# Kernel tuning notes

Measured on AMD Instinct MI355X. Metric: run time of the kernel, lower is better.

The kernel has to match this reference:

```python
import jax, jax.numpy as jnp
import numpy as np

SCALE = 1.0 / (100.0 ** 0.5)  # module hard-codes QK / sqrt(100)


def setup_inputs() -> dict:
    key = jax.random.key(0)
    k1, k2, k3 = jax.random.split(key, 3)
    B, S, D = 8, 2048, 512
    head_size = 64
    x = jax.random.normal(k1, (B, S, D), dtype=jnp.float32)
    kernel = jax.random.normal(k2, (3, D, head_size), dtype=jnp.float32) * 0.02
    dense = jax.random.normal(k3, (D, D), dtype=jnp.float32) * 0.02
    return {"x": x, "kernel": kernel, "dense": dense, "heads": 8}


def reference(x, kernel, dense, heads):
    # All heads use the SAME kernel slices in the original loop, so each
    # iteration produces an identical V; compute once and tile.
    WQ = jnp.einsum('bsd,dh->bsh', x, kernel[0])  # [B,S,Hd]
    WK = jnp.einsum('bsd,dh->bsh', x, kernel[1])
    WV = jnp.einsum('bsd,dh->bsh', x, kernel[2])
    scores = jnp.einsum('bqh,bkh->bqk', WQ, WK) * SCALE  # [B,S,S]
    attn = jax.nn.softmax(scores, axis=-1)
    V = jnp.einsum('bqk,bkh->bqh', attn, WV)  # [B,S,Hd]
    out = jnp.tile(V, (1, 1, heads))  # concat of identical heads -> [B,S,heads*Hd]
    return jnp.einsum('bsf,fo->bso', out, dense)
```

## Files before the change

kernel.cpp:

```cpp
#include <hip/hip_runtime.h>
#include <math.h>


typedef __bf16 bf16;
typedef __bf16 bf16x4v __attribute__((ext_vector_type(4)));
typedef __bf16 bf16x8v __attribute__((ext_vector_type(8)));
typedef float f32x4 __attribute__((ext_vector_type(4)));

namespace {
constexpr int kS = 2048;
constexpr int kD = 512;
constexpr int kRows = 16384;
}

#define MFMA16(a, b, c) __builtin_amdgcn_mfma_f32_16x16x32_bf16((a), (b), (c), 0, 0, 0)

__global__ __launch_bounds__(256) void prep_kernel(const float* __restrict__ w,
                                                   const float* __restrict__ dense,
                                                   bf16* __restrict__ wtg,
                                                   bf16* __restrict__ drt) {
  int idx = blockIdx.x * 256 + threadIdx.x;
  if (idx < 98304) {
    int mat = idx >> 15, rem = idx & 32767;
    int n = rem >> 9, k = rem & 511;
    wtg[idx] = (bf16)w[mat * 32768 + k * 64 + n];
  } else {
    int e = idx - 98304;
    int o = e >> 6, j = e & 63;
    float s = 0.f;
#pragma unroll
    for (int h = 0; h < 8; ++h) s += dense[(size_t)(h * 64 + j) * kD + o];
    drt[e] = (bf16)s;
  }
}

__global__ __launch_bounds__(256) void proj_kernel(const float* __restrict__ x,
                                                   const bf16* __restrict__ wtg,
                                                   bf16* __restrict__ wq,
                                                   bf16* __restrict__ wk,
                                                   bf16* __restrict__ wvt) {
  const int bt = blockIdx.x;
  const int tid = threadIdx.x;
  const int w = tid >> 6, tx = tid & 15, quad = (tid >> 4) & 3;
  const int row0 = bt * 64;

  __shared__ bf16 Xs[64 * 72];
  __shared__ bf16 Wts[3 * 64 * 72];

  f32x4 acc[3][4];
#pragma unroll
  for (int m = 0; m < 3; ++m)
#pragma unroll
    for (int nt = 0; nt < 4; ++nt) acc[m][nt] = (f32x4){0.f, 0.f, 0.f, 0.f};

  for (int k0 = 0; k0 < kD; k0 += 64) {
    __syncthreads();
#pragma unroll
    for (int p = 0; p < 4; ++p) {
      int i4 = tid + p * 256;
      int r = i4 >> 4, c4 = (i4 & 15) * 4;
      float4 f = *(const float4*)&x[(size_t)(row0 + r) * kD + k0 + c4];
      bf16x4v h = {(bf16)f.x, (bf16)f.y, (bf16)f.z, (bf16)f.w};
      *(bf16x4v*)&Xs[r * 72 + c4] = h;
    }
#pragma unroll
    for (int p = 0; p < 6; ++p) {
      int cc = tid + p * 256;
      int mat = cc >> 9, rem = cc & 511;
      int n = rem >> 3, c8 = (rem & 7) * 8;
      *(uint4*)&Wts[(mat * 64 + n) * 72 + c8] =
          *(const uint4*)&wtg[(size_t)mat * 32768 + (size_t)n * 512 + k0 + c8];
    }
    __syncthreads();
#pragma unroll
    for (int s = 0; s < 2; ++s) {
      bf16x8v a = *(bf16x8v*)&Xs[(w * 16 + tx) * 72 + s * 32 + quad * 8];
#pragma unroll
      for (int m = 0; m < 3; ++m)
#pragma unroll
        for (int nt = 0; nt < 4; ++nt) {
          bf16x8v bfr =
              *(bf16x8v*)&Wts[(m * 64 + nt * 16 + tx) * 72 + s * 32 + quad * 8];
          acc[m][nt] = MFMA16(a, bfr, acc[m][nt]);
        }
    }
  }

#pragma unroll
  for (int nt = 0; nt < 4; ++nt)
#pragma unroll
    for (int r = 0; r < 4; ++r) {
      int row_g = row0 + w * 16 + quad * 4 + r;
      int col = nt * 16 + tx;
      wq[(size_t)row_g * 64 + col] = (bf16)acc[0][nt][r];
      wk[(size_t)row_g * 64 + col] = (bf16)acc[1][nt][r];
    }
  __syncthreads();
  bf16* Vt = Xs;
#pragma unroll
  for (int nt = 0; nt < 4; ++nt)
#pragma unroll
    for (int r = 0; r < 4; ++r)
      Vt[(nt * 16 + tx) * 72 + (w * 16 + quad * 4 + r)] = (bf16)acc[2][nt][r];
  __syncthreads();
#pragma unroll
  for (int p = 0; p < 2; ++p) {
    int c = tid + p * 256;
    int v = c >> 3, seg = c & 7;
    *(uint4*)&wvt[(size_t)v * kRows + row0 + seg * 8] =
        *(uint4*)&Vt[v * 72 + seg * 8];
  }
}

__global__ __launch_bounds__(512, 4) void flash_kernel(
    const bf16* __restrict__ wq, const bf16* __restrict__ wk,
    const bf16* __restrict__ wvt, const bf16* __restrict__ drt,
    float* __restrict__ out) {
  const int bid = blockIdx.x;
  const int b = bid & 7, qb = bid >> 3;
  const int q0 = qb * 32;
  const int tid = threadIdx.x;
  const int w = tid >> 6, lane = tid & 63, tx = tid & 15, quad = (tid >> 4) & 3;

  __shared__ __align__(16) char lds[65536];
  __shared__ float Lsh[256];
  __shared__ __align__(16) bf16 vob[32 * 64];
  bf16* Ksw = (bf16*)(lds + w * 8192);
  bf16* Psw = Ksw;
  bf16* Vtw = (bf16*)(lds + w * 8192 + 4096);

  const bf16* wqb = wq + (size_t)(b * kS) * 64;
  const bf16* wkb = wk + (size_t)(b * kS) * 64;
  const bf16* wvb = wvt + b * kS;

  const int kc0 = (quad ^ (tx & 7)) * 8;
  const int kc1 = ((4 + quad) ^ (tx & 7)) * 8;
  const int h2 = (tx ^ (tx >> 2)) & 3;

  bf16x8v aq[2][2];
#pragma unroll
  for (int rt = 0; rt < 2; ++rt)
#pragma unroll
    for (int s = 0; s < 2; ++s)
      aq[rt][s] = *(const bf16x8v*)&wqb[(size_t)(q0 + rt * 16 + tx) * 64 +
                                        s * 32 + quad * 8];

  f32x4 oacc[2][4];
#pragma unroll
  for (int rt = 0; rt < 2; ++rt)
#pragma unroll
    for (int nt = 0; nt < 4; ++nt) oacc[rt][nt] = (f32x4){0.f, 0.f, 0.f, 0.f};
  float lsum[2][4] = {};

  const int ksr = lane >> 3, kslc = lane & 7;
  const int vsv = lane >> 2, vsck = lane & 3;

  for (int t = 0; t < 8; ++t) {
    const int k0 = (t * 8 + w) * 32;
#pragma unroll
    for (int j = 0; j < 4; ++j) {
      int r = ksr + j * 8;
      *(uint4*)&Ksw[r * 64 + ((kslc ^ (r & 7)) * 8)] =
          *(const uint4*)&wkb[(size_t)(k0 + r) * 64 + kslc * 8];
      int v = vsv + j * 16;
      *(uint4*)&Vtw[v * 32 + ((vsck ^ ((v ^ (v >> 2)) & 3)) * 8)] =
          *(const uint4*)&wvb[(size_t)v * kRows + k0 + vsck * 8];
    }

#pragma unroll
    for (int nt = 0; nt < 2; ++nt) {
      int krow = nt * 16 + tx;
      bf16x8v b0 = *(bf16x8v*)&Ksw[krow * 64 + kc0];
      bf16x8v b1 = *(bf16x8v*)&Ksw[krow * 64 + kc1];
#pragma unroll
      for (int rt = 0; rt < 2; ++rt) {
        f32x4 z = (f32x4){0.f, 0.f, 0.f, 0.f};
        z = MFMA16(aq[rt][0], b0, z);
        z = MFMA16(aq[rt][1], b1, z);
#pragma unroll
        for (int r = 0; r < 4; ++r) {
          float p = __expf(z[r] * 0.1f);
          lsum[rt][r] += p;
          int q = rt * 16 + quad * 4 + r;
          int chunk = nt * 2 + (tx >> 3);
          Psw[q * 32 + ((chunk ^ (r ^ quad)) * 8) + (tx & 7)] = (bf16)p;
        }
      }
    }

#pragma unroll
    for (int rt = 0; rt < 2; ++rt) {
      bf16x8v pa = *(bf16x8v*)&Psw[(rt * 16 + tx) * 32 + ((quad ^ h2) * 8)];
#pragma unroll
      for (int nt = 0; nt < 4; ++nt) {
        bf16x8v vb = *(bf16x8v*)&Vtw[(nt * 16 + tx) * 32 + ((quad ^ h2) * 8)];
        oacc[rt][nt] = MFMA16(pa, vb, oacc[rt][nt]);
      }
    }
  }

  __syncthreads();
  float* myO = (float*)(lds + w * 8192);
  float* myL = Lsh + w * 32;
#pragma unroll
  for (int rt = 0; rt < 2; ++rt)
#pragma unroll
    for (int nt = 0; nt < 4; ++nt)
#pragma unroll
      for (int r = 0; r < 4; ++r)
        myO[(rt * 16 + quad * 4 + r) * 64 + nt * 16 + tx] = oacc[rt][nt][r];
#pragma unroll
  for (int rt = 0; rt < 2; ++rt)
#pragma unroll
    for (int r = 0; r < 4; ++r) {
      float v = lsum[rt][r];
#pragma unroll
      for (int m = 1; m < 16; m <<= 1) v += __shfl_xor(v, m, 64);
      if (tx == 0) myL[rt * 16 + quad * 4 + r] = v;
    }
  __syncthreads();

#pragma unroll
  for (int p = 0; p < 4; ++p) {
    int e = tid + p * 512;
    int row = e >> 6, col = e & 63;
    float s = 0.f, lt = 0.f;
#pragma unroll
    for (int wv = 0; wv < 8; ++wv) {
      s += ((const float*)(lds + wv * 8192))[e];
      lt += Lsh[wv * 32 + row];
    }
    vob[row * 64 + (((col >> 3) ^ (row & 7)) * 8) + (col & 7)] = (bf16)(s / lt);
  }
  __syncthreads();

  bf16x8v av[2][2];
#pragma unroll
  for (int rt = 0; rt < 2; ++rt) {
    av[rt][0] = *(bf16x8v*)&vob[(rt * 16 + tx) * 64 + kc0];
    av[rt][1] = *(bf16x8v*)&vob[(rt * 16 + tx) * 64 + kc1];
  }

  float* OutS = (float*)lds;
#pragma unroll
  for (int c = 0; c < 2; ++c) {
    if (c) __syncthreads();
#pragma unroll
    for (int i = 0; i < 2; ++i) {
      const int ct = c * 16 + w * 2 + i;
      bf16x8v bd0 =
          *(const bf16x8v*)&drt[(size_t)(ct * 16 + tx) * 64 + quad * 8];
      bf16x8v bd1 =
          *(const bf16x8v*)&drt[(size_t)(ct * 16 + tx) * 64 + 32 + quad * 8];
#pragma unroll
      for (int rt = 0; rt < 2; ++rt) {
        f32x4 z = (f32x4){0.f, 0.f, 0.f, 0.f};
        z = MFMA16(av[rt][0], bd0, z);
        z = MFMA16(av[rt][1], bd1, z);
#pragma unroll
        for (int r = 0; r < 4; ++r)
          OutS[(rt * 16 + quad * 4 + r) * 260 + (w * 2 + i) * 16 + tx] = z[r];
      }
    }
    __syncthreads();
#pragma unroll
    for (int p = 0; p < 4; ++p) {
      int e = tid + p * 512;
      int row = e >> 6, seg = e & 63;
      *(float4*)&out[(size_t)(b * kS + q0 + row) * kD + c * 256 + seg * 4] =
          *(float4*)&OutS[row * 260 + seg * 4];
    }
  }
}

extern "C" void kernel_launch(void* const* d_in, const int* in_sizes, int n_in,
                              void* d_out, int out_size, void* d_ws,
                              size_t ws_size, hipStream_t stream) {
  const float* x = (const float*)d_in[0];
  const float* w = (const float*)d_in[1];
  const float* dense = (const float*)d_in[2];
  float* out = (float*)d_out;

  bf16* wq = (bf16*)d_ws;
  bf16* wk = wq + (size_t)kRows * 64;
  bf16* wvt = wk + (size_t)kRows * 64;
  bf16* wtg = wvt + (size_t)kRows * 64;
  bf16* drt = wtg + 98304;

  prep_kernel<<<512, 256, 0, stream>>>(w, dense, wtg, drt);
  proj_kernel<<<256, 256, 0, stream>>>(x, wtg, wq, wk, wvt);
  flash_kernel<<<512, 512, 0, stream>>>(wq, wk, wvt, drt, out);
}
```

Before: 137.7 us.

## Tile prep transposes, widen proj blocks, register-prefetch loads in proj and flash

The prep kernel now transposes the weights through a shared-memory tile and reduces the dense heads in registers, using 32 blocks instead of 512. The projection kernel runs 512 threads, with each wave computing 6 of the 12 output tiles, and prefetches the next K-slice of x and weights into registers while the current slice is computed. The flash kernel prefetches the next K/V tile into registers ahead of storing it to LDS, and hoists the swizzle offsets. This trades extra register pressure for latency hiding, and the flash loop issues one redundant wraparound load at the end.

```diff
diff --git a/kernel.cpp b/kernel.cpp
--- a/kernel.cpp
+++ b/kernel.cpp
@@ -19,22 +19,48 @@
                                                    const float* __restrict__ dense,
                                                    bf16* __restrict__ wtg,
                                                    bf16* __restrict__ drt) {
-  int idx = blockIdx.x * 256 + threadIdx.x;
-  if (idx < 98304) {
-    int mat = idx >> 15, rem = idx & 32767;
-    int n = rem >> 9, k = rem & 511;
-    wtg[idx] = (bf16)w[mat * 32768 + k * 64 + n];
+  const int bid = blockIdx.x, tid = threadIdx.x;
+  __shared__ float T[64][65];
+
+  if (bid < 24) {
+    const int mat = bid >> 3, k0 = (bid & 7) * 64;
+#pragma unroll
+    for (int p = 0; p < 16; ++p) {
+      int e = tid + p * 256;
+      int r = e >> 6, n = e & 63;
+      T[r][n] = w[mat * 32768 + (k0 + r) * 64 + n];
+    }
+    __syncthreads();
+#pragma unroll
+    for (int p = 0; p < 16; ++p) {
+      int e = tid + p * 256;
+      int n = e >> 6, c = e & 63;
+      wtg[(size_t)mat * 32768 + (size_t)n * 512 + k0 + c] = (bf16)T[c][n];
+    }
   } else {
-    int e = idx - 98304;
-    int o = e >> 6, j = e & 63;
-    float s = 0.f;
-#pragma unroll
-    for (int h = 0; h < 8; ++h) s += dense[(size_t)(h * 64 + j) * kD + o];
-    drt[e] = (bf16)s;
-  }
-}
-
-__global__ __launch_bounds__(256) void proj_kernel(const float* __restrict__ x,
+    const int o0 = (bid - 24) * 64;
+    const int oo = tid & 63, jg = tid >> 6;
+    float a[16];
+#pragma unroll
+    for (int i = 0; i < 16; ++i) a[i] = 0.f;
+#pragma unroll
+    for (int h = 0; h < 8; ++h)
+#pragma unroll
+      for (int i = 0; i < 16; ++i)
+        a[i] += dense[(size_t)(h * 64 + jg * 16 + i) * kD + o0 + oo];
+#pragma unroll
+    for (int i = 0; i < 16; ++i) T[oo][jg * 16 + i] = a[i];
+    __syncthreads();
+#pragma unroll
+    for (int p = 0; p < 16; ++p) {
+      int e = tid + p * 256;
+      int r = e >> 6, j = e & 63;
+      drt[(size_t)(o0 + r) * 64 + j] = (bf16)T[r][j];
+    }
+  }
+}
+
+__global__ __launch_bounds__(512) void proj_kernel(const float* __restrict__ x,
                                                    const bf16* __restrict__ wtg,
                                                    bf16* __restrict__ wq,
                                                    bf16* __restrict__ wk,
@@ -42,71 +68,92 @@
   const int bt = blockIdx.x;
   const int tid = threadIdx.x;
   const int w = tid >> 6, tx = tid & 15, quad = (tid >> 4) & 3;
+  const int rt = w & 3, nh = w >> 2;
   const int row0 = bt * 64;
 
   __shared__ bf16 Xs[64 * 72];
   __shared__ bf16 Wts[3 * 64 * 72];
 
-  f32x4 acc[3][4];
-#pragma unroll
-  for (int m = 0; m < 3; ++m)
-#pragma unroll
-    for (int nt = 0; nt < 4; ++nt) acc[m][nt] = (f32x4){0.f, 0.f, 0.f, 0.f};
-
+  f32x4 acc[6];
+#pragma unroll
+  for (int j = 0; j < 6; ++j) acc[j] = (f32x4){0.f, 0.f, 0.f, 0.f};
+
+  float4 xf[2];
+  uint4 wf[3];
+  auto proj_issue = [&](int K0) {
+#pragma unroll
+    for (int p = 0; p < 2; ++p) {
+      int i4 = tid + p * 512;
+      int r = i4 >> 4, c4 = (i4 & 15) * 4;
+      xf[p] = *(const float4*)&x[(size_t)(row0 + r) * kD + K0 + c4];
+    }
+#pragma unroll
+    for (int p = 0; p < 3; ++p) {
+      int cc = tid + p * 512;
+      int mat = cc >> 9, rem = cc & 511;
+      int n = rem >> 3, c8 = (rem & 7) * 8;
+      wf[p] = *(const uint4*)&wtg[(size_t)mat * 32768 + (size_t)n * 512 + K0 + c8];
+    }
+  };
+
+  proj_issue(0);
   for (int k0 = 0; k0 < kD; k0 += 64) {
     __syncthreads();
 #pragma unroll
-    for (int p = 0; p < 4; ++p) {
-      int i4 = tid + p * 256;
+    for (int p = 0; p < 2; ++p) {
+      int i4 = tid + p * 512;
       int r = i4 >> 4, c4 = (i4 & 15) * 4;
-      float4 f = *(const float4*)&x[(size_t)(row0 + r) * kD + k0 + c4];
+      float4 f = xf[p];
       bf16x4v h = {(bf16)f.x, (bf16)f.y, (bf16)f.z, (bf16)f.w};
       *(bf16x4v*)&Xs[r * 72 + c4] = h;
     }
 #pragma unroll
-    for (int p = 0; p < 6; ++p) {
-      int cc = tid + p * 256;
+    for (int p = 0; p < 3; ++p) {
+      int cc = tid + p * 512;
       int mat = cc >> 9, rem = cc & 511;
       int n = rem >> 3, c8 = (rem & 7) * 8;
-      *(uint4*)&Wts[(mat * 64 + n) * 72 + c8] =
-          *(const uint4*)&wtg[(size_t)mat * 32768 + (size_t)n * 512 + k0 + c8];
-    }
+      *(uint4*)&Wts[(mat * 64 + n) * 72 + c8] = wf[p];
+    }
+    if (k0 + 64 < kD) proj_issue(k0 + 64);
     __syncthreads();
 #pragma unroll
     for (int s = 0; s < 2; ++s) {
-      bf16x8v a = *(bf16x8v*)&Xs[(w * 16 + tx) * 72 + s * 32 + quad * 8];
-#pragma unroll
-      for (int m = 0; m < 3; ++m)
-#pragma unroll
-        for (int nt = 0; nt < 4; ++nt) {
-          bf16x8v bfr =
-              *(bf16x8v*)&Wts[(m * 64 + nt * 16 + tx) * 72 + s * 32 + quad * 8];
-          acc[m][nt] = MFMA16(a, bfr, acc[m][nt]);
-        }
-    }
-  }
-
-#pragma unroll
-  for (int nt = 0; nt < 4; ++nt)
-#pragma unroll
-    for (int r = 0; r < 4; ++r) {
-      int row_g = row0 + w * 16 + quad * 4 + r;
-      int col = nt * 16 + tx;
-      wq[(size_t)row_g * 64 + col] = (bf16)acc[0][nt][r];
-      wk[(size_t)row_g * 64 + col] = (bf16)acc[1][nt][r];
-    }
+      bf16x8v a = *(bf16x8v*)&Xs[(rt * 16 + tx) * 72 + s * 32 + quad * 8];
+#pragma unroll
+      for (int j = 0; j < 6; ++j) {
+        int ntg = nh * 6 + j;
+        bf16x8v bfr = *(bf16x8v*)&Wts[(ntg * 16 + tx) * 72 + s * 32 + quad * 8];
+        acc[j] = MFMA16(a, bfr, acc[j]);
+      }
+    }
+  }
+
+#pragma unroll
+  for (int j = 0; j < 6; ++j) {
+    int ntg = nh * 6 + j, mat = ntg >> 2, nt = ntg & 3;
+    if (mat < 2) {
+      bf16* dst = mat ? wk : wq;
+#pragma unroll
+      for (int r = 0; r < 4; ++r) {
+        int row_g = row0 + rt * 16 + quad * 4 + r;
+        dst[(size_t)row_g * 64 + nt * 16 + tx] = (bf16)acc[j][r];
+      }
+    }
+  }
   __syncthreads();
   bf16* Vt = Xs;
 #pragma unroll
-  for (int nt = 0; nt < 4; ++nt)
-#pragma unroll
-    for (int r = 0; r < 4; ++r)
-      Vt[(nt * 16 + tx) * 72 + (w * 16 + quad * 4 + r)] = (bf16)acc[2][nt][r];
-  __syncthreads();
-#pragma unroll
-  for (int p = 0; p < 2; ++p) {
-    int c = tid + p * 256;
-    int v = c >> 3, seg = c & 7;
+  for (int j = 0; j < 6; ++j) {
+    int ntg = nh * 6 + j, mat = ntg >> 2, nt = ntg & 3;
+    if (mat == 2) {
+#pragma unroll
+      for (int r = 0; r < 4; ++r)
+        Vt[(nt * 16 + tx) * 72 + rt * 16 + quad * 4 + r] = (bf16)acc[j][r];
+    }
+  }
+  __syncthreads();
+  {
+    int v = tid >> 3, seg = tid & 7;
     *(uint4*)&wvt[(size_t)v * kRows + row0 + seg * 8] =
         *(uint4*)&Vt[v * 72 + seg * 8];
   }
@@ -154,18 +201,27 @@
 
   const int ksr = lane >> 3, kslc = lane & 7;
   const int vsv = lane >> 2, vsck = lane & 3;
-
+  const int koff = (kslc ^ ksr) * 8;
+  const int voff = (vsck ^ ((vsv ^ (vsv >> 2)) & 3)) * 8;
+
+  uint4 kreg[4], vreg[4];
+  auto kv_issue = [&](int t) {
+    const int k0 = (t * 8 + w) * 32;
+#pragma unroll
+    for (int j = 0; j < 4; ++j) {
+      kreg[j] = *(const uint4*)&wkb[(size_t)(k0 + ksr + j * 8) * 64 + kslc * 8];
+      vreg[j] = *(const uint4*)&wvb[(size_t)(vsv + j * 16) * kRows + k0 + vsck * 8];
+    }
+  };
+
+  kv_issue(0);
   for (int t = 0; t < 8; ++t) {
-    const int k0 = (t * 8 + w) * 32;
 #pragma unroll
     for (int j = 0; j < 4; ++j) {
-      int r = ksr + j * 8;
-      *(uint4*)&Ksw[r * 64 + ((kslc ^ (r & 7)) * 8)] =
-          *(const uint4*)&wkb[(size_t)(k0 + r) * 64 + kslc * 8];
-      int v = vsv + j * 16;
-      *(uint4*)&Vtw[v * 32 + ((vsck ^ ((v ^ (v >> 2)) & 3)) * 8)] =
-          *(const uint4*)&wvb[(size_t)v * kRows + k0 + vsck * 8];
-    }
+      *(uint4*)&Ksw[(ksr + j * 8) * 64 + koff] = kreg[j];
+      *(uint4*)&Vtw[(vsv + j * 16) * 32 + voff] = vreg[j];
+    }
+    kv_issue((t + 1) & 7);
 
 #pragma unroll
     for (int nt = 0; nt < 2; ++nt) {
@@ -287,7 +343,7 @@
   bf16* wtg = wvt + (size_t)kRows * 64;
   bf16* drt = wtg + 98304;
 
-  prep_kernel<<<512, 256, 0, stream>>>(w, dense, wtg, drt);
-  proj_kernel<<<256, 256, 0, stream>>>(x, wtg, wq, wk, wvt);
+  prep_kernel<<<32, 256, 0, stream>>>(w, dense, wtg, drt);
+  proj_kernel<<<256, 512, 0, stream>>>(x, wtg, wq, wk, wvt);
   flash_kernel<<<512, 512, 0, stream>>>(wq, wk, wvt, drt, out);
 }
```

New measurement: 200.4 us. 1.46x slower.
